# Kernel optimization log

Hardware: AMD Instinct MI355X
Metric: run time of the kernel (lower is better)

The kernel has to match this reference:

```python
import jax, jax.numpy as jnp
import numpy as np
from jax import lax

B, H, W = 8, 64, 64
C = 192          # in_channel == out_channel
CI = 384         # inner_channel = int(2.0 * C)


def setup_inputs() -> dict:
    key = jax.random.key(0)
    ks = jax.random.split(key, 8)
    s = 0.02
    return {
        "x": jax.random.normal(ks[0], (B, H, W, C), jnp.float32),
        "Win": jax.random.normal(ks[1], (C, 2 * CI), jnp.float32) * s,
        "conv_w": jax.random.normal(ks[2], (CI, 1, 3, 3), jnp.float32) * s,
        "conv_b": jnp.zeros((CI,), jnp.float32),
        "Wout": jax.random.normal(ks[3], (CI, C), jnp.float32) * s,
        "Wm1": jax.random.normal(ks[4], (C, 4 * C), jnp.float32) * s,
        "bm1": jnp.zeros((4 * C,), jnp.float32),
        "Wm2": jax.random.normal(ks[5], (4 * C, C), jnp.float32) * s,
        "bm2": jnp.zeros((C,), jnp.float32),
    }


def reference(x, Win, conv_w, conv_b, Wout, Wm1, bm1, Wm2, bm2):
    silu = jax.nn.silu
    shortcut = x                                   # [B,H,W,C], norm1 is Identity (norm=None)
    xz = jnp.einsum('bhwc,cd->bhwd', x, Win)       # in_proj (no bias) -> [B,H,W,2*CI]
    x1, z = jnp.split(xz, 2, axis=-1)
    # channel_recover -> [B,CI,H,W], depthwise conv + silu
    xc = jnp.transpose(x1, (0, 3, 1, 2))
    xc = lax.conv_general_dilated(xc, conv_w, (1, 1), 'SAME',
                                  feature_group_count=CI,
                                  dimension_numbers=('NCHW', 'OIHW', 'NCHW'))
    xc = silu(xc + conv_b[None, :, None, None])
    L = H * W
    # cross_scan: K=2 views (row-major and transposed), doubled by flip_scan -> [B,4,CI,L]
    x0 = xc.reshape(B, CI, L)
    xt = jnp.transpose(xc, (0, 1, 3, 2)).reshape(B, CI, L)
    x_cross = jnp.stack([x0, xt], axis=1)
    xs = jnp.concatenate([x_cross, jnp.flip(x_cross, axis=-1)], axis=1)
    out_y = xs  # ssm() is abstract in MBaseBlock -> identity passthrough
    # scan_proj (CrossMerge): undo flips and permutations, sum branches
    inv_y = jnp.flip(out_y[:, 2:4], axis=-1)

    def unperm(v):  # branch scanned in transposed (W,H) order -> back to (H,W)
        return jnp.transpose(v.reshape(B, CI, W, H), (0, 1, 3, 2)).reshape(B, CI, L)

    y = out_y[:, 0] + inv_y[:, 0] + unperm(out_y[:, 1]) + unperm(inv_y[:, 1])
    y = jnp.transpose(y, (0, 2, 1)).reshape(B, H, W, CI)  # norm2 is Identity
    y = y * silu(z)                                       # gate
    out = jnp.einsum('bhwc,cd->bhwd', y, Wout)            # out_proj (no bias)
    out = shortcut + out                                  # dropout/drop_path are Identity
    # dense is Identity (in_channel == out_channel); MLP branch 192->768->192
    h = silu(jnp.einsum('bhwc,cd->bhwd', out, Wm1) + bm1)
    mlp = jnp.einsum('bhwd,dc->bhwc', h, Wm2) + bm2
    return out + mlp
```

## Files before the change

### kernel.cpp

```cpp
#include <hip/hip_runtime.h>
#include <hip/hip_bf16.h>

#define BDIM 8
#define HDIM 64
#define WDIM 64
#define CDIM 192
#define CIDIM 384
#define MTOK (BDIM * HDIM * WDIM)

using bf16 = __hip_bfloat16;
typedef __attribute__((ext_vector_type(8))) short short8;
typedef __attribute__((ext_vector_type(4))) float f32x4;

__device__ __forceinline__ float silu_f(float v) { return v / (1.0f + __expf(-v)); }
__device__ __forceinline__ float bf2f(short s) {
    union { unsigned u; float f; } x; x.u = ((unsigned)(unsigned short)s) << 16; return x.f;
}

__device__ __forceinline__ void gload_lds16(const bf16* g, bf16* l) {
    __builtin_amdgcn_global_load_lds(
        (const __attribute__((address_space(1))) void*)g,
        (__attribute__((address_space(3))) void*)l, 16, 0, 0);
}

template <int EPI, int NF>
__launch_bounds__(256, NF == 4 ? 2 : 4)
__global__ void gemm_mfma(const bf16* __restrict__ A, const bf16* __restrict__ BT,
                          const float* __restrict__ bias,
                          const float* __restrict__ residF,
                          const bf16* __restrict__ residB,
                          float* __restrict__ outF, bf16* __restrict__ outB,
                          bf16* __restrict__ outB2,
                          int M, int N, int K)
{
    constexpr int BN = 32 * NF;
    __shared__ bf16 As[128 * 64];
    __shared__ bf16 Bs[BN * 64];

    const int tid  = threadIdx.x;
    const int lane = tid & 63;
    const int wv   = tid >> 6;
    const int wm   = wv >> 1;
    const int wn   = wv & 1;
    const int m0   = blockIdx.y * 128;
    const int n0   = blockIdx.x * BN;

    const int srow  = lane >> 3;
    const int sslot = lane & 7;

    f32x4 acc[4][NF] = {};

    for (int k0 = 0; k0 < K; k0 += 64) {
        #pragma unroll
        for (int i = 0; i < 4; ++i) {
            const int rb = wv * 32 + i * 8;
            const int r  = rb + srow;
            gload_lds16(A + (size_t)(m0 + r) * K + k0 + ((sslot ^ (r & 7)) << 3),
                        &As[rb * 64]);
        }
        #pragma unroll
        for (int i = 0; i < NF; ++i) {
            const int rb = wv * (BN / 4) + i * 8;
            const int r  = rb + srow;
            gload_lds16(BT + (size_t)(n0 + r) * K + k0 + ((sslot ^ (r & 7)) << 3),
                        &Bs[rb * 64]);
        }
        __syncthreads();

        #pragma unroll
        for (int kk = 0; kk < 2; ++kk) {
            const int t = kk * 4 + (lane >> 4);
            short8 af[4], bfr[NF];
            #pragma unroll
            for (int mi = 0; mi < 4; ++mi) {
                const int m = wm * 64 + mi * 16 + (lane & 15);
                af[mi] = *reinterpret_cast<const short8*>(&As[m * 64 + ((t ^ (m & 7)) << 3)]);
            }
            #pragma unroll
            for (int ni = 0; ni < NF; ++ni) {
                const int n = wn * (16 * NF) + ni * 16 + (lane & 15);
                bfr[ni] = *reinterpret_cast<const short8*>(&Bs[n * 64 + ((t ^ (n & 7)) << 3)]);
            }
            #pragma unroll
            for (int mi = 0; mi < 4; ++mi)
                #pragma unroll
                for (int ni = 0; ni < NF; ++ni)
                    acc[mi][ni] = __builtin_amdgcn_mfma_f32_16x16x32_bf16(
                        af[mi], bfr[ni], acc[mi][ni], 0, 0, 0);
        }
        __syncthreads();
    }

    const int colb = n0 + wn * (16 * NF) + (lane & 15);
    const int rowb = m0 + wm * 64 + (lane >> 4) * 4;
    #pragma unroll
    for (int mi = 0; mi < 4; ++mi) {
        #pragma unroll
        for (int ni = 0; ni < NF; ++ni) {
            const int c = colb + ni * 16;
            #pragma unroll
            for (int j = 0; j < 4; ++j) {
                const int row = rowb + mi * 16 + j;
                const float v = acc[mi][ni][j];
                if constexpr (EPI == 0) {
                    if (c < CIDIM)
                        outB[(size_t)row * CIDIM + c] = __float2bfloat16(v);
                    else
                        outB2[(size_t)row * CIDIM + (c - CIDIM)] =
                            __float2bfloat16(4.0f * silu_f(v));
                } else if constexpr (EPI == 1) {
                    const size_t off = (size_t)row * N + c;
                    outB[off] = __float2bfloat16(v + residF[off]);
                } else if constexpr (EPI == 2) {
                    const size_t off = (size_t)row * N + c;
                    outB[off] = __float2bfloat16(silu_f(v + bias[c]));
                } else {
                    const size_t off = (size_t)row * N + c;
                    outF[off] = v + bias[c] + bf2f(*(const short*)&residB[off]);
                }
            }
        }
    }
}

__launch_bounds__(256)
__global__ void dwconv_gate_v6(const bf16* __restrict__ x1, const bf16* __restrict__ sz,
                               const float* __restrict__ wT, const float* __restrict__ conv_b,
                               bf16* __restrict__ y)
{
    const int bid = blockIdx.x;
    const int swz = (bid & 7) * ((int)gridDim.x >> 3) + (bid >> 3);
    const int f   = swz * 256 + threadIdx.x;
    const int m   = f / 48;
    const int cg  = f - m * 48;
    const int c0  = cg * 8;
    const int h   = (m >> 6) & 63;
    const int w   = m & 63;

    float acc[8];
    {
        const f32x4 ba = *reinterpret_cast<const f32x4*>(&conv_b[c0]);
        const f32x4 bb = *reinterpret_cast<const f32x4*>(&conv_b[c0 + 4]);
        acc[0] = ba[0]; acc[1] = ba[1]; acc[2] = ba[2]; acc[3] = ba[3];
        acc[4] = bb[0]; acc[5] = bb[1]; acc[6] = bb[2]; acc[7] = bb[3];
    }

    #pragma unroll
    for (int r = 0; r < 3; ++r) {
        const int hh = h + r - 1;
        if (hh < 0 || hh >= HDIM) continue;
        #pragma unroll
        for (int dw = 0; dw < 3; ++dw) {
            const int ww = w + dw - 1;
            if (ww < 0 || ww >= WDIM) continue;
            const int mm  = m + (r - 1) * WDIM + (dw - 1);
            const int tap = r * 3 + dw;
            const short8 t = *reinterpret_cast<const short8*>(&x1[(size_t)mm * CIDIM + c0]);
            const f32x4 wa = *reinterpret_cast<const f32x4*>(&wT[tap * CIDIM + c0]);
            const f32x4 wb = *reinterpret_cast<const f32x4*>(&wT[tap * CIDIM + c0 + 4]);
            acc[0] += bf2f(t[0]) * wa[0]; acc[1] += bf2f(t[1]) * wa[1];
            acc[2] += bf2f(t[2]) * wa[2]; acc[3] += bf2f(t[3]) * wa[3];
            acc[4] += bf2f(t[4]) * wb[0]; acc[5] += bf2f(t[5]) * wb[1];
            acc[6] += bf2f(t[6]) * wb[2]; acc[7] += bf2f(t[7]) * wb[3];
        }
    }

    const short8 g = *reinterpret_cast<const short8*>(&sz[(size_t)m * CIDIM + c0]);
    bf16 tmp[8];
    #pragma unroll
    for (int j = 0; j < 8; ++j)
        tmp[j] = __float2bfloat16(silu_f(acc[j]) * bf2f(g[j]));
    *reinterpret_cast<short8*>(&y[(size_t)m * CIDIM + c0]) =
        *reinterpret_cast<const short8*>(tmp);
}

#define SZ_WIN  (192 * 768)
#define SZ_WOUT (384 * 192)
#define SZ_WM1  (192 * 768)
#define SZ_WM2  (768 * 192)
#define SZ_CW   (CIDIM * 9)
#define XCVT    (MTOK * CDIM / 4)
#define SZ_ALL  (XCVT + SZ_WIN + SZ_WOUT + SZ_WM1 + SZ_WM2 + SZ_CW)

__launch_bounds__(256)
__global__ void prep_all(const float* __restrict__ x, const float* __restrict__ Win,
                         const float* __restrict__ Wout, const float* __restrict__ Wm1,
                         const float* __restrict__ Wm2, const float* __restrict__ convw,
                         bf16* __restrict__ xb, bf16* __restrict__ WinT,
                         bf16* __restrict__ WoutT, bf16* __restrict__ Wm1T,
                         bf16* __restrict__ Wm2T, float* __restrict__ wTc)
{
    int idx = blockIdx.x * 256 + threadIdx.x;
    if (idx < XCVT) {
        const int i = idx * 4;
        const float4 v = *reinterpret_cast<const float4*>(&x[i]);
        xb[i + 0] = __float2bfloat16(v.x);
        xb[i + 1] = __float2bfloat16(v.y);
        xb[i + 2] = __float2bfloat16(v.z);
        xb[i + 3] = __float2bfloat16(v.w);
        return;
    }
    idx -= XCVT;
    if (idx < SZ_WIN) {
        const int r = idx / 768, c = idx % 768;
        WinT[(size_t)c * 192 + r] = __float2bfloat16(Win[idx]);
        return;
    }
    idx -= SZ_WIN;
    if (idx < SZ_WOUT) {
        const int r = idx / 192, c = idx % 192;
        WoutT[(size_t)c * 384 + r] = __float2bfloat16(Wout[idx]);
        return;
    }
    idx -= SZ_WOUT;
    if (idx < SZ_WM1) {
        const int r = idx / 768, c = idx % 768;
        Wm1T[(size_t)c * 192 + r] = __float2bfloat16(Wm1[idx]);
        return;
    }
    idx -= SZ_WM1;
    if (idx < SZ_WM2) {
        const int r = idx / 192, c = idx % 192;
        Wm2T[(size_t)c * 768 + r] = __float2bfloat16(Wm2[idx]);
        return;
    }
    idx -= SZ_WM2;
    if (idx < SZ_CW) {
        const int ci = idx / 9, t = idx % 9;
        wTc[t * CIDIM + ci] = convw[idx];
    }
}

extern "C" void kernel_launch(void* const* d_in, const int* in_sizes, int n_in,
                              void* d_out, int out_size, void* d_ws, size_t ws_size,
                              hipStream_t stream)
{
    const float* x      = (const float*)d_in[0];
    const float* Win    = (const float*)d_in[1];
    const float* conv_w = (const float*)d_in[2];
    const float* conv_b = (const float*)d_in[3];
    const float* Wout   = (const float*)d_in[4];
    const float* Wm1    = (const float*)d_in[5];
    const float* bm1    = (const float*)d_in[6];
    const float* Wm2    = (const float*)d_in[7];
    const float* bm2    = (const float*)d_in[8];
    float* out = (float*)d_out;

    char* ws = (char*)d_ws;
    size_t o = 0;
    bf16*  xb    = (bf16*)(ws + o); o += (size_t)MTOK * CDIM * 2;
    bf16*  WinT  = (bf16*)(ws + o); o += (size_t)768 * 192 * 2;
    bf16*  WoutT = (bf16*)(ws + o); o += (size_t)192 * 384 * 2;
    bf16*  Wm1T  = (bf16*)(ws + o); o += (size_t)768 * 192 * 2;
    bf16*  Wm2T  = (bf16*)(ws + o); o += (size_t)192 * 768 * 2;
    float* wTc   = (float*)(ws + o); o += (size_t)9 * CIDIM * 4;
    bf16*  ws_x1 = (bf16*)(ws + o); o += (size_t)MTOK * CIDIM * 2;
    bf16*  ws_sz = (bf16*)(ws + o); o += (size_t)MTOK * CIDIM * 2;
    bf16*  ws_y  = (bf16*)(ws + o); o += (size_t)MTOK * CIDIM * 2;
    bf16*  ws_ob = (bf16*)(ws + o); o += (size_t)MTOK * CDIM * 2;
    bf16*  ws_h  = ws_x1;

    prep_all<<<dim3((SZ_ALL + 255) / 256), dim3(256), 0, stream>>>(
        x, Win, Wout, Wm1, Wm2, conv_w, xb, WinT, WoutT, Wm1T, Wm2T, wTc);

    gemm_mfma<0, 4><<<dim3(768 / 128, MTOK / 128), dim3(256), 0, stream>>>(
        xb, WinT, nullptr, nullptr, nullptr, nullptr, ws_x1, ws_sz, MTOK, 768, CDIM);

    dwconv_gate_v6<<<dim3(MTOK * 48 / 256), dim3(256), 0, stream>>>(
        ws_x1, ws_sz, wTc, conv_b, ws_y);

    gemm_mfma<1, 2><<<dim3(192 / 64, MTOK / 128), dim3(256), 0, stream>>>(
        ws_y, WoutT, nullptr, x, nullptr, nullptr, ws_ob, nullptr, MTOK, CDIM, CIDIM);

    gemm_mfma<2, 4><<<dim3(768 / 128, MTOK / 128), dim3(256), 0, stream>>>(
        ws_ob, Wm1T, bm1, nullptr, nullptr, nullptr, ws_h, nullptr, MTOK, 768, CDIM);

    gemm_mfma<3, 2><<<dim3(192 / 64, MTOK / 128), dim3(256), 0, stream>>>(
        ws_h, Wm2T, bm2, nullptr, ws_ob, out, nullptr, nullptr, MTOK, CDIM, 768);
}
```

Measured before the change: 141.9 us.

## Add single-shot K=192 GEMM kernel with 64x64 tiles and XCD-aware block swizzle

Adds a specialized GEMM for the two K=192 projections that loads the full 64x192 A and B panels into LDS once, removing the k-loop and its per-step barriers, and uses 64x64 output tiles to launch many more blocks. The general GEMM is specialized to a 128x64 tile, and both kernels use a 1D grid with a bid&7 swizzle so neighbouring M tiles land on the same XCD for L2 reuse of B. The trade-off is more redundant reloading of A across the 12 N-tiles and larger LDS use (48KB) per block, which may limit occupancy.

```diff
diff --git a/kernel.cpp b/kernel.cpp
--- a/kernel.cpp
+++ b/kernel.cpp
@@ -23,80 +23,71 @@
         (__attribute__((address_space(3))) void*)l, 16, 0, 0);
 }
 
-template <int EPI, int NF>
-__launch_bounds__(256, NF == 4 ? 2 : 4)
-__global__ void gemm_mfma(const bf16* __restrict__ A, const bf16* __restrict__ BT,
+template <int EPI>
+__launch_bounds__(256, 3)
+__global__ void gemm_k192(const bf16* __restrict__ A, const bf16* __restrict__ BT,
                           const float* __restrict__ bias,
-                          const float* __restrict__ residF,
-                          const bf16* __restrict__ residB,
-                          float* __restrict__ outF, bf16* __restrict__ outB,
-                          bf16* __restrict__ outB2,
-                          int M, int N, int K)
-{
-    constexpr int BN = 32 * NF;
-    __shared__ bf16 As[128 * 64];
-    __shared__ bf16 Bs[BN * 64];
+                          bf16* __restrict__ outB, bf16* __restrict__ outB2,
+                          int N, int NX)
+{
+    __shared__ bf16 As[64 * 192];
+    __shared__ bf16 Bs[64 * 192];
+
+    const int bid = blockIdx.x;
+    const int c8  = bid & 7;
+    const int kk_ = bid >> 3;
+    const int bx  = kk_ % NX;
+    const int by  = (kk_ / NX) * 8 + c8;
+    const int m0  = by * 64;
+    const int n0  = bx * 64;
 
     const int tid  = threadIdx.x;
     const int lane = tid & 63;
     const int wv   = tid >> 6;
     const int wm   = wv >> 1;
     const int wn   = wv & 1;
-    const int m0   = blockIdx.y * 128;
-    const int n0   = blockIdx.x * BN;
-
-    const int srow  = lane >> 3;
-    const int sslot = lane & 7;
-
-    f32x4 acc[4][NF] = {};
-
-    for (int k0 = 0; k0 < K; k0 += 64) {
-        #pragma unroll
-        for (int i = 0; i < 4; ++i) {
-            const int rb = wv * 32 + i * 8;
-            const int r  = rb + srow;
-            gload_lds16(A + (size_t)(m0 + r) * K + k0 + ((sslot ^ (r & 7)) << 3),
-                        &As[rb * 64]);
-        }
-        #pragma unroll
-        for (int i = 0; i < NF; ++i) {
-            const int rb = wv * (BN / 4) + i * 8;
-            const int r  = rb + srow;
-            gload_lds16(BT + (size_t)(n0 + r) * K + k0 + ((sslot ^ (r & 7)) << 3),
-                        &Bs[rb * 64]);
-        }
-        __syncthreads();
-
-        #pragma unroll
-        for (int kk = 0; kk < 2; ++kk) {
-            const int t = kk * 4 + (lane >> 4);
-            short8 af[4], bfr[NF];
-            #pragma unroll
-            for (int mi = 0; mi < 4; ++mi) {
-                const int m = wm * 64 + mi * 16 + (lane & 15);
-                af[mi] = *reinterpret_cast<const short8*>(&As[m * 64 + ((t ^ (m & 7)) << 3)]);
-            }
-            #pragma unroll
-            for (int ni = 0; ni < NF; ++ni) {
-                const int n = wn * (16 * NF) + ni * 16 + (lane & 15);
-                bfr[ni] = *reinterpret_cast<const short8*>(&Bs[n * 64 + ((t ^ (n & 7)) << 3)]);
-            }
-            #pragma unroll
-            for (int mi = 0; mi < 4; ++mi)
-                #pragma unroll
-                for (int ni = 0; ni < NF; ++ni)
-                    acc[mi][ni] = __builtin_amdgcn_mfma_f32_16x16x32_bf16(
-                        af[mi], bfr[ni], acc[mi][ni], 0, 0, 0);
-        }
-        __syncthreads();
-    }
-
-    const int colb = n0 + wn * (16 * NF) + (lane & 15);
-    const int rowb = m0 + wm * 64 + (lane >> 4) * 4;
-    #pragma unroll
-    for (int mi = 0; mi < 4; ++mi) {
-        #pragma unroll
-        for (int ni = 0; ni < NF; ++ni) {
+
+    #pragma unroll
+    for (int i = 0; i < 6; ++i) {
+        const int ci   = wv * 6 + i;
+        const int c    = ci * 64 + lane;
+        const int row  = c / 24;
+        const int slot = c - row * 24;
+        const int lsl  = slot ^ (row & 7);
+        gload_lds16(A  + (size_t)(m0 + row) * 192 + lsl * 8, &As[ci * 512]);
+        gload_lds16(BT + (size_t)(n0 + row) * 192 + lsl * 8, &Bs[ci * 512]);
+    }
+    __syncthreads();
+
+    f32x4 acc[2][2] = {};
+    #pragma unroll
+    for (int ks = 0; ks < 6; ++ks) {
+        const int t = ks * 4 + (lane >> 4);
+        short8 af[2], bfr[2];
+        #pragma unroll
+        for (int mi = 0; mi < 2; ++mi) {
+            const int m = wm * 32 + mi * 16 + (lane & 15);
+            af[mi] = *reinterpret_cast<const short8*>(&As[m * 192 + ((t ^ (m & 7)) << 3)]);
+        }
+        #pragma unroll
+        for (int ni = 0; ni < 2; ++ni) {
+            const int n = wn * 32 + ni * 16 + (lane & 15);
+            bfr[ni] = *reinterpret_cast<const short8*>(&Bs[n * 192 + ((t ^ (n & 7)) << 3)]);
+        }
+        #pragma unroll
+        for (int mi = 0; mi < 2; ++mi)
+            #pragma unroll
+            for (int ni = 0; ni < 2; ++ni)
+                acc[mi][ni] = __builtin_amdgcn_mfma_f32_16x16x32_bf16(
+                    af[mi], bfr[ni], acc[mi][ni], 0, 0, 0);
+    }
+
+    const int colb = n0 + wn * 32 + (lane & 15);
+    const int rowb = m0 + wm * 32 + (lane >> 4) * 4;
+    #pragma unroll
+    for (int mi = 0; mi < 2; ++mi) {
+        #pragma unroll
+        for (int ni = 0; ni < 2; ++ni) {
             const int c = colb + ni * 16;
             #pragma unroll
             for (int j = 0; j < 4; ++j) {
@@ -108,14 +99,101 @@
                     else
                         outB2[(size_t)row * CIDIM + (c - CIDIM)] =
                             __float2bfloat16(4.0f * silu_f(v));
-                } else if constexpr (EPI == 1) {
-                    const size_t off = (size_t)row * N + c;
+                } else {
+                    outB[(size_t)row * N + c] = __float2bfloat16(silu_f(v + bias[c]));
+                }
+            }
+        }
+    }
+}
+
+template <int EPI>
+__launch_bounds__(256, 4)
+__global__ void gemm_mfma(const bf16* __restrict__ A, const bf16* __restrict__ BT,
+                          const float* __restrict__ bias,
+                          const float* __restrict__ residF,
+                          const bf16* __restrict__ residB,
+                          float* __restrict__ outF, bf16* __restrict__ outB,
+                          int M, int N, int K, int NX)
+{
+    __shared__ bf16 As[128 * 64];
+    __shared__ bf16 Bs[64 * 64];
+
+    const int bid = blockIdx.x;
+    const int c8  = bid & 7;
+    const int kq  = bid >> 3;
+    const int bx  = kq % NX;
+    const int by  = (kq / NX) * 8 + c8;
+    const int m0  = by * 128;
+    const int n0  = bx * 64;
+
+    const int tid  = threadIdx.x;
+    const int lane = tid & 63;
+    const int wv   = tid >> 6;
+    const int wm   = wv >> 1;
+    const int wn   = wv & 1;
+
+    const int srow  = lane >> 3;
+    const int sslot = lane & 7;
+
+    f32x4 acc[4][2] = {};
+
+    for (int k0 = 0; k0 < K; k0 += 64) {
+        #pragma unroll
+        for (int i = 0; i < 4; ++i) {
+            const int rb = wv * 32 + i * 8;
+            const int r  = rb + srow;
+            gload_lds16(A + (size_t)(m0 + r) * K + k0 + ((sslot ^ (r & 7)) << 3),
+                        &As[rb * 64]);
+        }
+        #pragma unroll
+        for (int i = 0; i < 2; ++i) {
+            const int rb = wv * 16 + i * 8;
+            const int r  = rb + srow;
+            gload_lds16(BT + (size_t)(n0 + r) * K + k0 + ((sslot ^ (r & 7)) << 3),
+                        &Bs[rb * 64]);
+        }
+        __syncthreads();
+
+        #pragma unroll
+        for (int kk = 0; kk < 2; ++kk) {
+            const int t = kk * 4 + (lane >> 4);
+            short8 af[4], bfr[2];
+            #pragma unroll
+            for (int mi = 0; mi < 4; ++mi) {
+                const int m = wm * 64 + mi * 16 + (lane & 15);
+                af[mi] = *reinterpret_cast<const short8*>(&As[m * 64 + ((t ^ (m & 7)) << 3)]);
+            }
+            #pragma unroll
+            for (int ni = 0; ni < 2; ++ni) {
+                const int n = wn * 32 + ni * 16 + (lane & 15);
+                bfr[ni] = *reinterpret_cast<const short8*>(&Bs[n * 64 + ((t ^ (n & 7)) << 3)]);
+            }
+            #pragma unroll
+            for (int mi = 0; mi < 4; ++mi)
+                #pragma unroll
+                for (int ni = 0; ni < 2; ++ni)
+                    acc[mi][ni] = __builtin_amdgcn_mfma_f32_16x16x32_bf16(
+                        af[mi], bfr[ni], acc[mi][ni], 0, 0, 0);
+        }
+        __syncthreads();
+    }
+
+    const int colb = n0 + wn * 32 + (lane & 15);
+    const int rowb = m0 + wm * 64 + (lane >> 4) * 4;
+    #pragma unroll
+    for (int mi = 0; mi < 4; ++mi) {
+        #pragma unroll
+        for (int ni = 0; ni < 2; ++ni) {
+            const int c = colb + ni * 16;
+            #pragma unroll
+            for (int j = 0; j < 4; ++j) {
+                const int row = rowb + mi * 16 + j;
+                const size_t off = (size_t)row * N + c;
+                const float v = acc[mi][ni][j];
+                if constexpr (EPI == 1) {
                     outB[off] = __float2bfloat16(v + residF[off]);
-                } else if constexpr (EPI == 2) {
-                    const size_t off = (size_t)row * N + c;
-                    outB[off] = __float2bfloat16(silu_f(v + bias[c]));
                 } else {
-                    const size_t off = (size_t)row * N + c;
                     outF[off] = v + bias[c] + bf2f(*(const short*)&residB[off]);
                 }
             }
@@ -263,18 +341,18 @@
     prep_all<<<dim3((SZ_ALL + 255) / 256), dim3(256), 0, stream>>>(
         x, Win, Wout, Wm1, Wm2, conv_w, xb, WinT, WoutT, Wm1T, Wm2T, wTc);
 
-    gemm_mfma<0, 4><<<dim3(768 / 128, MTOK / 128), dim3(256), 0, stream>>>(
-        xb, WinT, nullptr, nullptr, nullptr, nullptr, ws_x1, ws_sz, MTOK, 768, CDIM);
+    gemm_k192<0><<<dim3(12 * 512), dim3(256), 0, stream>>>(
+        xb, WinT, nullptr, ws_x1, ws_sz, 768, 12);
 
     dwconv_gate_v6<<<dim3(MTOK * 48 / 256), dim3(256), 0, stream>>>(
         ws_x1, ws_sz, wTc, conv_b, ws_y);
 
-    gemm_mfma<1, 2><<<dim3(192 / 64, MTOK / 128), dim3(256), 0, stream>>>(
-        ws_y, WoutT, nullptr, x, nullptr, nullptr, ws_ob, nullptr, MTOK, CDIM, CIDIM);
-
-    gemm_mfma<2, 4><<<dim3(768 / 128, MTOK / 128), dim3(256), 0, stream>>>(
-        ws_ob, Wm1T, bm1, nullptr, nullptr, nullptr, ws_h, nullptr, MTOK, 768, CDIM);
-
-    gemm_mfma<3, 2><<<dim3(192 / 64, MTOK / 128), dim3(256), 0, stream>>>(
-        ws_h, Wm2T, bm2, nullptr, ws_ob, out, nullptr, nullptr, MTOK, CDIM, 768);
-}
+    gemm_mfma<1><<<dim3(3 * 256), dim3(256), 0, stream>>>(
+        ws_y, WoutT, nullptr, x, nullptr, nullptr, ws_ob, MTOK, CDIM, CIDIM, 3);
+
+    gemm_k192<2><<<dim3(12 * 512), dim3(256), 0, stream>>>(
+        ws_ob, Wm1T, bm1, ws_h, nullptr, 768, 12);
+
+    gemm_mfma<3><<<dim3(3 * 256), dim3(256), 0, stream>>>(
+        ws_h, Wm2T, bm2, nullptr, ws_ob, out, nullptr, MTOK, CDIM, 768, 3);
+}
```

Result: faster. 124.1 us (-12.6%).
